# Kernel tuning notes

Measured on AMD Instinct MI355X. Metric: run time of the kernel, lower is better.

Reference implementation:

```python
import jax, jax.numpy as jnp
import numpy as np

B = 4
CTX = 2048
N_SUB = 16
RANK = 16
RANK_T = 16
LATENT = 256           # int(sqrt(CTX * N_SUB * 2))
T = 2 + 2 * RANK_T     # 34 transformation channels
H = 768
WD = 768
EPS = 1e-12
ASYM = 1e-4


def bgn(x):
    # backward_gradient_normalization: identity in the forward pass
    return x


def siglog(x):
    return jnp.sign(x) * jnp.log1p(jnp.abs(x))


def cmul(a, b):
    re = a[..., 0] * b[..., 0] - a[..., 1] * b[..., 1]
    im = a[..., 0] * b[..., 1] + a[..., 1] * b[..., 0]
    return jnp.stack([re, im], axis=-1)


def cdiv(a, b, eps):
    den = jnp.maximum(b[..., 0] ** 2 + b[..., 1] ** 2, eps)
    re = (a[..., 0] * b[..., 0] + a[..., 1] * b[..., 1]) / den
    im = (a[..., 1] * b[..., 0] - a[..., 0] * b[..., 1]) / den
    return jnp.stack([re, im], axis=-1)


def interp_linear(x, out_size):
    # x: [B, C, L] -> [B, C, out_size]; torch 'linear', align_corners=False
    L = x.shape[-1]
    pos = (jnp.arange(out_size, dtype=jnp.float32) + 0.5) * (L / out_size) - 0.5
    pos = jnp.clip(pos, 0.0, L - 1)
    lo = jnp.floor(pos).astype(jnp.int32)
    hi = jnp.minimum(lo + 1, L - 1)
    w = (pos - lo).astype(x.dtype)
    return x[..., lo] * (1.0 - w) + x[..., hi] * w


def transform_space(space, shift, z, size):
    # space [1,C,R,size,2], shift [B,C,R,2], z [B,Rt,C,R,2]
    sp = space + shift[:, :, :, None, :]
    bz = shift.shape[0]
    zt = jnp.transpose(z, (0, 4, 2, 3, 1)).reshape(bz, 2 * N_SUB * RANK, RANK_T)
    zt = interp_linear(zt, size)
    zt = jnp.transpose(zt.reshape(bz, 2, N_SUB, RANK, size), (0, 2, 3, 4, 1))
    return cmul(sp, zt)


def _forward(x, Wc, bc, space_i, space_j, inversions, G_Re, G_Im, w_mix, projections):
    xt = bgn(x @ Wc.T + bc)                        # [B, 4*LATENT]
    sl = LATENT * 2
    xm = (xt[:, :sl] * siglog(xt[:, sl:])).reshape(-1, LATENT, 2)
    GR, GI = bgn(G_Re), bgn(G_Im)
    xr, xi = xm[..., 0], xm[..., 1]
    Re = jnp.einsum('bl,tclr->btcr', xr, GR) - jnp.einsum('bl,tclr->btcr', xi, GI)
    Im = jnp.einsum('bl,tclr->btcr', xr, GI) + jnp.einsum('bl,tclr->btcr', xi, GR)
    shp = (Re.shape[0], T, N_SUB, LATENT, RANK)
    Re = bgn(jnp.broadcast_to(Re[:, :, :, None, :], shp))
    Im = bgn(jnp.broadcast_to(Im[:, :, :, None, :], shp))
    mag = jnp.sqrt(Re ** 2 + Im ** 2 + EPS)
    cos_t, sin_t = Re / mag, Im / mag
    msum = mag.sum(axis=3) + EPS
    cos_w = (cos_t * mag).sum(axis=3) / msum
    sin_w = (sin_t * mag).sum(axis=3) / msum
    mm = mag.mean(axis=3)
    trans = jnp.stack([cos_w * mm, sin_w * mm], axis=-1)   # [B,T,C,R,2]
    si = transform_space(bgn(space_i), trans[:, 0], trans[:, 2:2 + RANK_T], H)
    sj = transform_space(bgn(space_j), trans[:, 1], trans[:, 2 + RANK_T:2 + 2 * RANK_T], WD)
    inv = bgn(inversions)
    gI = cmul(si, inv)                                      # [B,C,R,H,2]
    gJ = cdiv(jnp.broadcast_to(inv, sj.shape), sj, ASYM)    # [B,C,R,W,2]
    wm = bgn(w_mix)
    tRe = jnp.einsum('bl,lk->bk', xr, wm[..., 0]) - jnp.einsum('bl,lk->bk', xi, wm[..., 1])
    tIm = jnp.einsum('bl,lk->bk', xr, wm[..., 1]) + jnp.einsum('bl,lk->bk', xi, wm[..., 0])
    beta = jax.nn.softmax(jnp.sqrt(tRe ** 2 + tIm ** 2 + EPS).reshape(-1, N_SUB, RANK), axis=-1)
    beta = beta[..., None, None]
    gI = (beta * gI).sum(axis=2)                            # [B,C,H,2]
    gJ = (beta * gJ).sum(axis=2)                            # [B,C,W,2]
    w_Re = jnp.einsum('bch,bcw->bchw', gI[..., 0], gJ[..., 0]) - jnp.einsum('bch,bcw->bchw', gI[..., 1], gJ[..., 1])
    w_Im = jnp.einsum('bch,bcw->bchw', gI[..., 0], gJ[..., 1]) + jnp.einsum('bch,bcw->bchw', gI[..., 1], gJ[..., 0])
    proj = bgn(projections)
    den = jnp.sqrt(jnp.sum(proj ** 2, axis=-1) + EPS)       # [1,C,H,W]
    pc, ps = proj[..., 0] / den, proj[..., 1] / den
    weights = w_Re * pc + w_Im * ps                         # [B,C,H,W]
    return weights.sum(axis=1)                              # [B,H,W]


def setup_inputs() -> dict:
    key = jax.random.key(0)
    ks = jax.random.split(key, 12)
    lim = 1.0 / np.sqrt(CTX)
    x = jax.random.normal(ks[0], (B, CTX), jnp.float32)
    Wc = jax.random.uniform(ks[1], (LATENT * 4, CTX), jnp.float32, -lim, lim)
    bc = jax.random.uniform(ks[2], (LATENT * 4,), jnp.float32, -lim, lim)
    space_i = jax.random.uniform(ks[3], (1, N_SUB, RANK, H, 2), jnp.float32, -1.0, 1.0)
    space_j = jax.random.uniform(ks[4], (1, N_SUB, RANK, WD, 2), jnp.float32, -1.0, 1.0)
    inversions = jax.random.uniform(ks[5], (1, N_SUB, 1, 1, 2), jnp.float32, -1.0, 1.0)
    gx = float(np.sqrt(6.0 / (N_SUB * LATENT * RANK + T * LATENT * RANK)))
    G_Re = jax.random.uniform(ks[6], (T, N_SUB, LATENT, RANK), jnp.float32, -gx, gx)
    G_Im = jax.random.uniform(ks[7], (T, N_SUB, LATENT, RANK), jnp.float32, -gx, gx)
    w_mix = jnp.stack([jnp.ones((LATENT, N_SUB * RANK), jnp.float32),
                       jnp.zeros((LATENT, N_SUB * RANK), jnp.float32)], axis=-1)
    pr = jax.random.gamma(ks[8], 0.5, (1, N_SUB, H, WD))
    pr = pr / (jnp.sum(pr, axis=-1, keepdims=True))         # Dirichlet(0.5) over last dim
    pi = jax.random.normal(ks[9], (1, N_SUB, H, WD)) * 0.001
    projections = jnp.stack([pr, pi], axis=-1).astype(jnp.float32)
    return {"x": x, "Wc": Wc, "bc": bc, "space_i": space_i, "space_j": space_j,
            "inversions": inversions, "G_Re": G_Re, "G_Im": G_Im,
            "w_mix": w_mix, "projections": projections}


def reference(x, Wc, bc, space_i, space_j, inversions, G_Re, G_Im, w_mix, projections):
    return _forward(x, Wc, bc, space_i, space_j, inversions, G_Re, G_Im, w_mix, projections)
```

## Files before the change

kernel.cpp:

```cpp
#include <hip/hip_runtime.h>
#include <math.h>

#define NCTX 2048
#define NT 34

typedef float f4 __attribute__((ext_vector_type(4)));
typedef float f2 __attribute__((ext_vector_type(2)));

#define OFF_XR 0u
#define OFF_XI 1024u
#define OFF_TR 2048u
#define OFF_GI 71680u
#define OFF_GJ 169984u

__device__ __forceinline__ float siglog(float v) {
  return copysignf(log1pf(fabsf(v)), v);
}

__device__ __forceinline__ f4 ntload4(const float* p) {
  return __builtin_nontemporal_load((const f4*)p);
}

__global__ __launch_bounds__(256) void k1_xm(const float* __restrict__ x,
                                             const float* __restrict__ Wc,
                                             const float* __restrict__ bc,
                                             float* __restrict__ xr,
                                             float* __restrict__ xi) {
  const int p = blockIdx.x;
  const int tid = threadIdx.x;
  const float* w1 = Wc + (size_t)p * NCTX;
  const float* w2 = Wc + (size_t)(p + 512) * NCTX;
  const f4* x4 = (const f4*)x;
  float a00 = 0.f, a01 = 0.f, a02 = 0.f, a03 = 0.f;
  float a10 = 0.f, a11 = 0.f, a12 = 0.f, a13 = 0.f;
  #pragma unroll
  for (int it = 0; it < 2; ++it) {
    int i = tid + it * 256;
    f4 wa = ntload4(w1 + i * 4);
    f4 wb = ntload4(w2 + i * 4);
    f4 v0 = x4[i];
    f4 v1 = x4[512 + i];
    f4 v2 = x4[1024 + i];
    f4 v3 = x4[1536 + i];
    a00 += wa.x * v0.x + wa.y * v0.y + wa.z * v0.z + wa.w * v0.w;
    a01 += wa.x * v1.x + wa.y * v1.y + wa.z * v1.z + wa.w * v1.w;
    a02 += wa.x * v2.x + wa.y * v2.y + wa.z * v2.z + wa.w * v2.w;
    a03 += wa.x * v3.x + wa.y * v3.y + wa.z * v3.z + wa.w * v3.w;
    a10 += wb.x * v0.x + wb.y * v0.y + wb.z * v0.z + wb.w * v0.w;
    a11 += wb.x * v1.x + wb.y * v1.y + wb.z * v1.z + wb.w * v1.w;
    a12 += wb.x * v2.x + wb.y * v2.y + wb.z * v2.z + wb.w * v2.w;
    a13 += wb.x * v3.x + wb.y * v3.y + wb.z * v3.z + wb.w * v3.w;
  }
  __shared__ float red[8][256];
  __shared__ float sums[8];
  red[0][tid] = a00; red[1][tid] = a01; red[2][tid] = a02; red[3][tid] = a03;
  red[4][tid] = a10; red[5][tid] = a11; red[6][tid] = a12; red[7][tid] = a13;
  __syncthreads();
  const int wv = tid >> 6, lane = tid & 63;
  #pragma unroll
  for (int q = 0; q < 2; ++q) {
    int combo = wv * 2 + q;
    float s = red[combo][lane] + red[combo][lane + 64] +
              red[combo][lane + 128] + red[combo][lane + 192];
    #pragma unroll
    for (int off = 32; off > 0; off >>= 1) s += __shfl_down(s, off, 64);
    if (lane == 0) sums[combo] = s;
  }
  __syncthreads();
  if (tid < 4) {
    float d1 = sums[tid] + bc[p];
    float d2 = sums[4 + tid] + bc[p + 512];
    float v = d1 * siglog(d2);
    float* dst = (p & 1) ? xi : xr;
    dst[tid * 256 + (p >> 1)] = v;
  }
}

__global__ __launch_bounds__(256) void k3_trans(const float* __restrict__ GR,
                                                const float* __restrict__ GIm,
                                                const float* __restrict__ xr,
                                                const float* __restrict__ xi,
                                                float* __restrict__ tr) {
  const int t = blockIdx.x >> 4;
  const int c = blockIdx.x & 15;
  const int tid = threadIdx.x;
  __shared__ float grT[16][260];
  __shared__ float giT[16][260];
  __shared__ float xr_s[1024];
  __shared__ float xi_s[1024];
  __shared__ float2 red2[4][64];
  const float* grp = GR + (size_t)(t * 16 + c) * 4096;
  const float* gip = GIm + (size_t)(t * 16 + c) * 4096;
  #pragma unroll
  for (int it = 0; it < 4; ++it) {
    int k = tid + it * 256;
    int l = k >> 2, q = (k & 3) * 4;
    f4 g = ntload4(grp + k * 4);
    grT[q + 0][l] = g.x; grT[q + 1][l] = g.y; grT[q + 2][l] = g.z; grT[q + 3][l] = g.w;
    f4 h = ntload4(gip + k * 4);
    giT[q + 0][l] = h.x; giT[q + 1][l] = h.y; giT[q + 2][l] = h.z; giT[q + 3][l] = h.w;
  }
  ((f4*)xr_s)[tid] = ((const f4*)xr)[tid];
  ((f4*)xi_s)[tid] = ((const f4*)xi)[tid];
  __syncthreads();
  const int r = tid & 15, b = (tid >> 4) & 3, lseg = tid >> 6;
  const f4* grv = (const f4*)&grT[r][lseg * 64];
  const f4* giv = (const f4*)&giT[r][lseg * 64];
  const f4* xrv = (const f4*)&xr_s[b * 256 + lseg * 64];
  const f4* xiv = (const f4*)&xi_s[b * 256 + lseg * 64];
  float are = 0.f, aim = 0.f;
  #pragma unroll
  for (int li = 0; li < 16; ++li) {
    f4 g = grv[li], gg = giv[li], vr = xrv[li], vi = xiv[li];
    are += vr.x * g.x - vi.x * gg.x;  aim += vr.x * gg.x + vi.x * g.x;
    are += vr.y * g.y - vi.y * gg.y;  aim += vr.y * gg.y + vi.y * g.y;
    are += vr.z * g.z - vi.z * gg.z;  aim += vr.z * gg.z + vi.z * g.z;
    are += vr.w * g.w - vi.w * gg.w;  aim += vr.w * gg.w + vi.w * g.w;
  }
  red2[lseg][b * 16 + r] = make_float2(are, aim);
  __syncthreads();
  if (tid < 64) {
    const int rr = tid & 15, bb = tid >> 4;
    float2 s0 = red2[0][tid], s1 = red2[1][tid], s2 = red2[2][tid], s3 = red2[3][tid];
    float sre = s0.x + s1.x + s2.x + s3.x;
    float sim = s0.y + s1.y + s2.y + s3.y;
    float mag = sqrtf(sre * sre + sim * sim + 1e-12f);
    float scale = 256.f * mag / (256.f * mag + 1e-12f);
    size_t o = ((((size_t)bb * NT + t) * 16 + c) * 16 + rr) * 2;
    tr[o]     = sre * scale;
    tr[o + 1] = sim * scale;
  }
}

__global__ __launch_bounds__(256) void k5_g(const float* __restrict__ space_i,
                                            const float* __restrict__ space_j,
                                            const float* __restrict__ invs,
                                            const float* __restrict__ tr,
                                            const float* __restrict__ xr,
                                            const float* __restrict__ xi,
                                            const float* __restrict__ wm,
                                            float* __restrict__ gI,
                                            float* __restrict__ gJ) {
  const int c = blockIdx.x, b = blockIdx.y;
  const int which = blockIdx.z / 3, seg = blockIdx.z % 3;
  const int tid = threadIdx.x;
  __shared__ float xr_s[256], xi_s[256];
  __shared__ float2 redb[16][16];
  __shared__ float sh_beta[16];
  __shared__ float sh_shift[16][2];
  __shared__ float sh_z[16][16][2];
  xr_s[tid] = xr[b * 256 + tid];
  xi_s[tid] = xi[b * 256 + tid];
  if (tid < 32) {
    int r = tid >> 1, comp = tid & 1;
    sh_shift[r][comp] = tr[((((size_t)b * NT + which) * 16 + c) * 16 + r) * 2 + comp];
  }
  for (int idx = tid; idx < 512; idx += 256) {
    int rt = idx >> 5, r = (idx >> 1) & 15, comp = idx & 1;
    int t = 2 + which * 16 + rt;
    sh_z[rt][r][comp] = tr[((((size_t)b * NT + t) * 16 + c) * 16 + r) * 2 + comp];
  }
  __syncthreads();
  {
    const int r = tid & 15, lseg = tid >> 4;
    const float2* wm2 = (const float2*)wm;
    float tre = 0.f, tim = 0.f;
    #pragma unroll
    for (int li = 0; li < 16; ++li) {
      int l = lseg * 16 + li;
      float2 w = wm2[(size_t)l * 256 + c * 16 + r];
      float vr = xr_s[l], vi = xi_s[l];
      tre += vr * w.x - vi * w.y;
      tim += vr * w.y + vi * w.x;
    }
    redb[lseg][r] = make_float2(tre, tim);
  }
  __syncthreads();
  if (tid < 16) {
    float sr = 0.f, si = 0.f;
    #pragma unroll
    for (int s = 0; s < 16; ++s) { sr += redb[s][tid].x; si += redb[s][tid].y; }
    float val = sqrtf(sr * sr + si * si + 1e-12f);
    float m = val;
    #pragma unroll
    for (int off = 8; off > 0; off >>= 1) m = fmaxf(m, __shfl_xor(m, off, 16));
    float e = expf(val - m);
    float ss = e;
    #pragma unroll
    for (int off = 8; off > 0; off >>= 1) ss += __shfl_xor(ss, off, 16);
    sh_beta[tid] = e / ss;
  }
  const float inv_re = invs[c * 2], inv_im = invs[c * 2 + 1];
  __syncthreads();
  const float2* sp2 = (const float2*)(which == 0 ? space_i : space_j);
  sp2 += (size_t)c * 16 * 768;
  float2* gout = (float2*)(which == 0 ? gI : gJ);
  gout += (size_t)(b * 16 + c) * 768;
  const int h = seg * 256 + tid;
  float pos = ((float)h + 0.5f) * (16.f / 768.f) - 0.5f;
  pos = fminf(fmaxf(pos, 0.f), 15.f);
  int lo = (int)floorf(pos);
  int hi = min(lo + 1, 15);
  float w = pos - (float)lo;
  float accR = 0.f, accI = 0.f;
  #pragma unroll
  for (int r = 0; r < 16; ++r) {
    float2 sp = sp2[r * 768 + h];
    float spr = sp.x + sh_shift[r][0];
    float spi = sp.y + sh_shift[r][1];
    float ztr = sh_z[lo][r][0] * (1.f - w) + sh_z[hi][r][0] * w;
    float zti = sh_z[lo][r][1] * (1.f - w) + sh_z[hi][r][1] * w;
    float sre = spr * ztr - spi * zti;
    float sim = spr * zti + spi * ztr;
    float br = sh_beta[r];
    if (which == 0) {
      accR += br * sre;
      accI += br * sim;
    } else {
      float den = fmaxf(sre * sre + sim * sim, 1e-4f);
      float id = 1.f / den;
      accR += br * (inv_re * sre + inv_im * sim) * id;
      accI += br * (inv_im * sre - inv_re * sim) * id;
    }
  }
  float2 o;
  if (which == 0) {
    o.x = accR * inv_re - accI * inv_im;
    o.y = accR * inv_im + accI * inv_re;
  } else {
    o.x = accR; o.y = accI;
  }
  gout[h] = o;
}

__global__ __launch_bounds__(256) void k6_out(const float* __restrict__ proj,
                                              const float* __restrict__ gI,
                                              const float* __restrict__ gJ,
                                              float* __restrict__ out) {
  const int w0 = blockIdx.x * 32;
  const int h0 = blockIdx.y * 32;
  const int tid = threadIdx.x;
  const int tw = tid & 15, th = tid >> 4;
  __shared__ float2 gIs[64][32];
  __shared__ float2 gJs[64][32];
  const float2* gI2 = (const float2*)gI;
  const float2* gJ2 = (const float2*)gJ;
  #pragma unroll
  for (int it = 0; it < 8; ++it) {
    int idx = tid + it * 256;
    int i = idx & 31, bcp = idx >> 5;
    gIs[bcp][i] = gI2[(size_t)bcp * 768 + h0 + i];
    gJs[bcp][i] = gJ2[(size_t)bcp * 768 + w0 + i];
  }
  __syncthreads();
  const float* pp = proj + ((size_t)(h0 + th * 2) * 384 + (w0 >> 1) + tw) * 4;
  float acc[4][4];
  #pragma unroll
  for (int b = 0; b < 4; ++b)
    #pragma unroll
    for (int q = 0; q < 4; ++q) acc[b][q] = 0.f;

  f4 pa = ntload4(pp);
  f4 pb = ntload4(pp + 384 * 4);
  #pragma unroll 1
  for (int c = 0; c < 16; ++c) {
    f4 c0 = pa, c1 = pb;
    if (c < 15) {
      size_t nxt = (size_t)(c + 1) * 768 * 384 * 4;
      pa = ntload4(pp + nxt);
      pb = ntload4(pp + nxt + 384 * 4);
    }
    float rq00 = rsqrtf(c0.x * c0.x + c0.y * c0.y + 1e-12f);
    float rq01 = rsqrtf(c0.z * c0.z + c0.w * c0.w + 1e-12f);
    float rq10 = rsqrtf(c1.x * c1.x + c1.y * c1.y + 1e-12f);
    float rq11 = rsqrtf(c1.z * c1.z + c1.w * c1.w + 1e-12f);
    float pr00 = c0.x * rq00, pi00 = c0.y * rq00;
    float pr01 = c0.z * rq01, pi01 = c0.w * rq01;
    float pr10 = c1.x * rq10, pi10 = c1.y * rq10;
    float pr11 = c1.z * rq11, pi11 = c1.w * rq11;
    #pragma unroll
    for (int b = 0; b < 4; ++b) {
      float2 gi0 = gIs[b * 16 + c][th * 2];
      float2 gi1 = gIs[b * 16 + c][th * 2 + 1];
      float2 gj0 = gJs[b * 16 + c][tw * 2];
      float2 gj1 = gJs[b * 16 + c][tw * 2 + 1];
      acc[b][0] += (gi0.x * gj0.x - gi0.y * gj0.y) * pr00 + (gi0.x * gj0.y + gi0.y * gj0.x) * pi00;
      acc[b][1] += (gi0.x * gj1.x - gi0.y * gj1.y) * pr01 + (gi0.x * gj1.y + gi0.y * gj1.x) * pi01;
      acc[b][2] += (gi1.x * gj0.x - gi1.y * gj0.y) * pr10 + (gi1.x * gj0.y + gi1.y * gj0.x) * pi10;
      acc[b][3] += (gi1.x * gj1.x - gi1.y * gj1.y) * pr11 + (gi1.x * gj1.y + gi1.y * gj1.x) * pi11;
    }
  }
  #pragma unroll
  for (int b = 0; b < 4; ++b) {
    #pragma unroll
    for (int hh = 0; hh < 2; ++hh) {
      int h = h0 + th * 2 + hh;
      f2 st;
      st.x = acc[b][hh * 2 + 0];
      st.y = acc[b][hh * 2 + 1];
      __builtin_nontemporal_store(st,
          (f2*)(out + (((size_t)b * 768 + h) * 384 + (w0 >> 1) + tw) * 2));
    }
  }
}

extern "C" void kernel_launch(void* const* d_in, const int* in_sizes, int n_in,
                              void* d_out, int out_size, void* d_ws, size_t ws_size,
                              hipStream_t stream) {
  (void)in_sizes; (void)n_in; (void)out_size; (void)ws_size;
  const float* x    = (const float*)d_in[0];
  const float* Wc   = (const float*)d_in[1];
  const float* bc   = (const float*)d_in[2];
  const float* spi  = (const float*)d_in[3];
  const float* spj  = (const float*)d_in[4];
  const float* invs = (const float*)d_in[5];
  const float* GR   = (const float*)d_in[6];
  const float* GIm  = (const float*)d_in[7];
  const float* wm   = (const float*)d_in[8];
  const float* proj = (const float*)d_in[9];
  float* out = (float*)d_out;
  float* ws  = (float*)d_ws;

  k1_xm   <<<512, 256, 0, stream>>>(x, Wc, bc, ws + OFF_XR, ws + OFF_XI);
  k3_trans<<<NT * 16, 256, 0, stream>>>(GR, GIm, ws + OFF_XR, ws + OFF_XI, ws + OFF_TR);
  k5_g    <<<dim3(16, 4, 6), 256, 0, stream>>>(spi, spj, invs, ws + OFF_TR,
                                               ws + OFF_XR, ws + OFF_XI, wm,
                                               ws + OFF_GI, ws + OFF_GJ);
  k6_out  <<<dim3(24, 24), 256, 0, stream>>>(proj, ws + OFF_GI, ws + OFF_GJ, out);
}
```

Baseline: 42.90 us.

## Fuse g-vector generation into output kernel and merge beta into trans kernel

Removes the separate k5_g kernel. The beta softmax computation now runs as extra blocks of the transformation kernel, and each output tile recomputes its own gI/gJ slices per channel from space, tr and beta held in shared memory. This saves one launch and the gI/gJ round trip through global memory. In exchange, every one of the 576 output blocks redundantly reloads tr per channel, adds two syncthreads per channel iteration, and recomputes the space products. The proj prefetch depth grows to two channels ahead.

```diff
diff --git a/kernel.cpp b/kernel.cpp
--- a/kernel.cpp
+++ b/kernel.cpp
@@ -10,8 +10,7 @@
 #define OFF_XR 0u
 #define OFF_XI 1024u
 #define OFF_TR 2048u
-#define OFF_GI 71680u
-#define OFF_GJ 169984u
+#define OFF_BE 71680u
 
 __device__ __forceinline__ float siglog(float v) {
   return copysignf(log1pf(fabsf(v)), v);
@@ -21,7 +20,7 @@
   return __builtin_nontemporal_load((const f4*)p);
 }
 
-__global__ __launch_bounds__(256) void k1_xm(const float* __restrict__ x,
+__global__ __launch_bounds__(256) void n1_xm(const float* __restrict__ x,
                                              const float* __restrict__ Wc,
                                              const float* __restrict__ bc,
                                              float* __restrict__ xr,
@@ -76,220 +75,240 @@
   }
 }
 
-__global__ __launch_bounds__(256) void k3_trans(const float* __restrict__ GR,
-                                                const float* __restrict__ GIm,
-                                                const float* __restrict__ xr,
-                                                const float* __restrict__ xi,
-                                                float* __restrict__ tr) {
-  const int t = blockIdx.x >> 4;
-  const int c = blockIdx.x & 15;
+__global__ __launch_bounds__(256) void n2_trans_beta(
+    const float* __restrict__ GR, const float* __restrict__ GIm,
+    const float* __restrict__ xr, const float* __restrict__ xi,
+    const float* __restrict__ wm, float* __restrict__ tr,
+    float* __restrict__ beta) {
+  const int u = blockIdx.x;
   const int tid = threadIdx.x;
-  __shared__ float grT[16][260];
-  __shared__ float giT[16][260];
-  __shared__ float xr_s[1024];
-  __shared__ float xi_s[1024];
-  __shared__ float2 red2[4][64];
-  const float* grp = GR + (size_t)(t * 16 + c) * 4096;
-  const float* gip = GIm + (size_t)(t * 16 + c) * 4096;
-  #pragma unroll
-  for (int it = 0; it < 4; ++it) {
-    int k = tid + it * 256;
-    int l = k >> 2, q = (k & 3) * 4;
-    f4 g = ntload4(grp + k * 4);
-    grT[q + 0][l] = g.x; grT[q + 1][l] = g.y; grT[q + 2][l] = g.z; grT[q + 3][l] = g.w;
-    f4 h = ntload4(gip + k * 4);
-    giT[q + 0][l] = h.x; giT[q + 1][l] = h.y; giT[q + 2][l] = h.z; giT[q + 3][l] = h.w;
-  }
-  ((f4*)xr_s)[tid] = ((const f4*)xr)[tid];
-  ((f4*)xi_s)[tid] = ((const f4*)xi)[tid];
-  __syncthreads();
-  const int r = tid & 15, b = (tid >> 4) & 3, lseg = tid >> 6;
-  const f4* grv = (const f4*)&grT[r][lseg * 64];
-  const f4* giv = (const f4*)&giT[r][lseg * 64];
-  const f4* xrv = (const f4*)&xr_s[b * 256 + lseg * 64];
-  const f4* xiv = (const f4*)&xi_s[b * 256 + lseg * 64];
-  float are = 0.f, aim = 0.f;
-  #pragma unroll
-  for (int li = 0; li < 16; ++li) {
-    f4 g = grv[li], gg = giv[li], vr = xrv[li], vi = xiv[li];
-    are += vr.x * g.x - vi.x * gg.x;  aim += vr.x * gg.x + vi.x * g.x;
-    are += vr.y * g.y - vi.y * gg.y;  aim += vr.y * gg.y + vi.y * g.y;
-    are += vr.z * g.z - vi.z * gg.z;  aim += vr.z * gg.z + vi.z * g.z;
-    are += vr.w * g.w - vi.w * gg.w;  aim += vr.w * gg.w + vi.w * g.w;
-  }
-  red2[lseg][b * 16 + r] = make_float2(are, aim);
-  __syncthreads();
-  if (tid < 64) {
-    const int rr = tid & 15, bb = tid >> 4;
-    float2 s0 = red2[0][tid], s1 = red2[1][tid], s2 = red2[2][tid], s3 = red2[3][tid];
-    float sre = s0.x + s1.x + s2.x + s3.x;
-    float sim = s0.y + s1.y + s2.y + s3.y;
-    float mag = sqrtf(sre * sre + sim * sim + 1e-12f);
-    float scale = 256.f * mag / (256.f * mag + 1e-12f);
-    size_t o = ((((size_t)bb * NT + t) * 16 + c) * 16 + rr) * 2;
-    tr[o]     = sre * scale;
-    tr[o + 1] = sim * scale;
-  }
-}
-
-__global__ __launch_bounds__(256) void k5_g(const float* __restrict__ space_i,
-                                            const float* __restrict__ space_j,
-                                            const float* __restrict__ invs,
-                                            const float* __restrict__ tr,
-                                            const float* __restrict__ xr,
-                                            const float* __restrict__ xi,
-                                            const float* __restrict__ wm,
-                                            float* __restrict__ gI,
-                                            float* __restrict__ gJ) {
-  const int c = blockIdx.x, b = blockIdx.y;
-  const int which = blockIdx.z / 3, seg = blockIdx.z % 3;
-  const int tid = threadIdx.x;
-  __shared__ float xr_s[256], xi_s[256];
-  __shared__ float2 redb[16][16];
-  __shared__ float sh_beta[16];
-  __shared__ float sh_shift[16][2];
-  __shared__ float sh_z[16][16][2];
-  xr_s[tid] = xr[b * 256 + tid];
-  xi_s[tid] = xi[b * 256 + tid];
-  if (tid < 32) {
-    int r = tid >> 1, comp = tid & 1;
-    sh_shift[r][comp] = tr[((((size_t)b * NT + which) * 16 + c) * 16 + r) * 2 + comp];
-  }
-  for (int idx = tid; idx < 512; idx += 256) {
-    int rt = idx >> 5, r = (idx >> 1) & 15, comp = idx & 1;
-    int t = 2 + which * 16 + rt;
-    sh_z[rt][r][comp] = tr[((((size_t)b * NT + t) * 16 + c) * 16 + r) * 2 + comp];
-  }
-  __syncthreads();
-  {
+  __shared__ __align__(16) float smem[10880];
+  if (u < NT * 16) {
+    const int t = u >> 4;
+    const int c = u & 15;
+    float* grT = smem;
+    float* giT = smem + 4160;
+    float* xr_s = smem + 8320;
+    float* xi_s = smem + 9344;
+    f2* red2 = (f2*)(smem + 10368);
+    const float* grp = GR + (size_t)(t * 16 + c) * 4096;
+    const float* gip = GIm + (size_t)(t * 16 + c) * 4096;
+    #pragma unroll
+    for (int it = 0; it < 4; ++it) {
+      int k = tid + it * 256;
+      int l = k >> 2, q = (k & 3) * 4;
+      f4 g = ntload4(grp + k * 4);
+      grT[(q + 0) * 260 + l] = g.x; grT[(q + 1) * 260 + l] = g.y;
+      grT[(q + 2) * 260 + l] = g.z; grT[(q + 3) * 260 + l] = g.w;
+      f4 h = ntload4(gip + k * 4);
+      giT[(q + 0) * 260 + l] = h.x; giT[(q + 1) * 260 + l] = h.y;
+      giT[(q + 2) * 260 + l] = h.z; giT[(q + 3) * 260 + l] = h.w;
+    }
+    ((f4*)xr_s)[tid] = ((const f4*)xr)[tid];
+    ((f4*)xi_s)[tid] = ((const f4*)xi)[tid];
+    __syncthreads();
+    const int r = tid & 15, b = (tid >> 4) & 3, lseg = tid >> 6;
+    const f4* grv = (const f4*)&grT[r * 260 + lseg * 64];
+    const f4* giv = (const f4*)&giT[r * 260 + lseg * 64];
+    const f4* xrv = (const f4*)&xr_s[b * 256 + lseg * 64];
+    const f4* xiv = (const f4*)&xi_s[b * 256 + lseg * 64];
+    float are = 0.f, aim = 0.f;
+    #pragma unroll
+    for (int li = 0; li < 16; ++li) {
+      f4 g = grv[li], gg = giv[li], vr = xrv[li], vi = xiv[li];
+      are += vr.x * g.x - vi.x * gg.x;  aim += vr.x * gg.x + vi.x * g.x;
+      are += vr.y * g.y - vi.y * gg.y;  aim += vr.y * gg.y + vi.y * g.y;
+      are += vr.z * g.z - vi.z * gg.z;  aim += vr.z * gg.z + vi.z * g.z;
+      are += vr.w * g.w - vi.w * gg.w;  aim += vr.w * gg.w + vi.w * g.w;
+    }
+    f2 rv; rv.x = are; rv.y = aim;
+    red2[lseg * 64 + b * 16 + r] = rv;
+    __syncthreads();
+    if (tid < 64) {
+      const int rr = tid & 15, bb = tid >> 4;
+      f2 s0 = red2[0 * 64 + tid], s1 = red2[1 * 64 + tid];
+      f2 s2 = red2[2 * 64 + tid], s3 = red2[3 * 64 + tid];
+      float sre = s0.x + s1.x + s2.x + s3.x;
+      float sim = s0.y + s1.y + s2.y + s3.y;
+      float mag = sqrtf(sre * sre + sim * sim + 1e-12f);
+      float scale = 256.f * mag / (256.f * mag + 1e-12f);
+      size_t o = ((((size_t)bb * NT + t) * 16 + c) * 16 + rr) * 2;
+      tr[o]     = sre * scale;
+      tr[o + 1] = sim * scale;
+    }
+  } else {
+    const int u2 = u - NT * 16;
+    const int n = u2 & 15, b = u2 >> 4;
+    float* xr_s = smem;
+    float* xi_s = smem + 256;
+    f2* redb = (f2*)(smem + 512);
+    {
+      int l = tid;
+      xr_s[l] = xr[b * 256 + l];
+      xi_s[l] = xi[b * 256 + l];
+    }
+    __syncthreads();
     const int r = tid & 15, lseg = tid >> 4;
-    const float2* wm2 = (const float2*)wm;
+    const f2* wm2 = (const f2*)wm;
     float tre = 0.f, tim = 0.f;
     #pragma unroll
     for (int li = 0; li < 16; ++li) {
       int l = lseg * 16 + li;
-      float2 w = wm2[(size_t)l * 256 + c * 16 + r];
+      f2 w = wm2[(size_t)l * 256 + n * 16 + r];
       float vr = xr_s[l], vi = xi_s[l];
       tre += vr * w.x - vi * w.y;
       tim += vr * w.y + vi * w.x;
     }
-    redb[lseg][r] = make_float2(tre, tim);
-  }
-  __syncthreads();
-  if (tid < 16) {
-    float sr = 0.f, si = 0.f;
-    #pragma unroll
-    for (int s = 0; s < 16; ++s) { sr += redb[s][tid].x; si += redb[s][tid].y; }
-    float val = sqrtf(sr * sr + si * si + 1e-12f);
-    float m = val;
-    #pragma unroll
-    for (int off = 8; off > 0; off >>= 1) m = fmaxf(m, __shfl_xor(m, off, 16));
-    float e = expf(val - m);
-    float ss = e;
-    #pragma unroll
-    for (int off = 8; off > 0; off >>= 1) ss += __shfl_xor(ss, off, 16);
-    sh_beta[tid] = e / ss;
-  }
-  const float inv_re = invs[c * 2], inv_im = invs[c * 2 + 1];
-  __syncthreads();
-  const float2* sp2 = (const float2*)(which == 0 ? space_i : space_j);
-  sp2 += (size_t)c * 16 * 768;
-  float2* gout = (float2*)(which == 0 ? gI : gJ);
-  gout += (size_t)(b * 16 + c) * 768;
-  const int h = seg * 256 + tid;
-  float pos = ((float)h + 0.5f) * (16.f / 768.f) - 0.5f;
-  pos = fminf(fmaxf(pos, 0.f), 15.f);
-  int lo = (int)floorf(pos);
-  int hi = min(lo + 1, 15);
-  float w = pos - (float)lo;
-  float accR = 0.f, accI = 0.f;
-  #pragma unroll
-  for (int r = 0; r < 16; ++r) {
-    float2 sp = sp2[r * 768 + h];
-    float spr = sp.x + sh_shift[r][0];
-    float spi = sp.y + sh_shift[r][1];
-    float ztr = sh_z[lo][r][0] * (1.f - w) + sh_z[hi][r][0] * w;
-    float zti = sh_z[lo][r][1] * (1.f - w) + sh_z[hi][r][1] * w;
-    float sre = spr * ztr - spi * zti;
-    float sim = spr * zti + spi * ztr;
-    float br = sh_beta[r];
-    if (which == 0) {
-      accR += br * sre;
-      accI += br * sim;
-    } else {
-      float den = fmaxf(sre * sre + sim * sim, 1e-4f);
-      float id = 1.f / den;
-      accR += br * (inv_re * sre + inv_im * sim) * id;
-      accI += br * (inv_im * sre - inv_re * sim) * id;
-    }
-  }
-  float2 o;
-  if (which == 0) {
-    o.x = accR * inv_re - accI * inv_im;
-    o.y = accR * inv_im + accI * inv_re;
-  } else {
-    o.x = accR; o.y = accI;
-  }
-  gout[h] = o;
-}
-
-__global__ __launch_bounds__(256) void k6_out(const float* __restrict__ proj,
-                                              const float* __restrict__ gI,
-                                              const float* __restrict__ gJ,
-                                              float* __restrict__ out) {
-  const int w0 = blockIdx.x * 32;
-  const int h0 = blockIdx.y * 32;
+    f2 rv; rv.x = tre; rv.y = tim;
+    redb[lseg * 16 + r] = rv;
+    __syncthreads();
+    if (tid < 16) {
+      float sr = 0.f, si = 0.f;
+      #pragma unroll
+      for (int s = 0; s < 16; ++s) { sr += redb[s * 16 + tid].x; si += redb[s * 16 + tid].y; }
+      float val = sqrtf(sr * sr + si * si + 1e-12f);
+      float m = val;
+      #pragma unroll
+      for (int off = 8; off > 0; off >>= 1) m = fmaxf(m, __shfl_xor(m, off, 16));
+      float e = expf(val - m);
+      float ss = e;
+      #pragma unroll
+      for (int off = 8; off > 0; off >>= 1) ss += __shfl_xor(ss, off, 16);
+      beta[(b * 16 + n) * 16 + tid] = e / ss;
+    }
+  }
+}
+
+__global__ __launch_bounds__(256) void n3_out(
+    const float* __restrict__ space_i, const float* __restrict__ space_j,
+    const float* __restrict__ invs, const float* __restrict__ tr,
+    const float* __restrict__ beta, const float* __restrict__ proj,
+    float* __restrict__ out) {
+  const int u = blockIdx.x;
+  const int w0 = (u % 24) * 32;
+  const int h0 = (u / 24) * 32;
   const int tid = threadIdx.x;
   const int tw = tid & 15, th = tid >> 4;
-  __shared__ float2 gIs[64][32];
-  __shared__ float2 gJs[64][32];
-  const float2* gI2 = (const float2*)gI;
-  const float2* gJ2 = (const float2*)gJ;
-  #pragma unroll
-  for (int it = 0; it < 8; ++it) {
-    int idx = tid + it * 256;
-    int i = idx & 31, bcp = idx >> 5;
-    gIs[bcp][i] = gI2[(size_t)bcp * 768 + h0 + i];
-    gJs[bcp][i] = gJ2[(size_t)bcp * 768 + w0 + i];
-  }
-  __syncthreads();
-  const float* pp = proj + ((size_t)(h0 + th * 2) * 384 + (w0 >> 1) + tw) * 4;
+  __shared__ f2 lds_tr[4][NT][16];
+  __shared__ float lds_beta[4][16][16];
+  __shared__ f2 lds_inv[16];
+  __shared__ f2 gIt[4][32];
+  __shared__ f2 gJt[4][32];
+
+  for (int idx = tid; idx < 1024; idx += 256) lds_beta[idx >> 8][(idx >> 4) & 15][idx & 15] = beta[idx];
+  if (tid < 16) lds_inv[tid] = ((const f2*)invs)[tid];
+
   float acc[4][4];
   #pragma unroll
   for (int b = 0; b < 4; ++b)
     #pragma unroll
     for (int q = 0; q < 4; ++q) acc[b][q] = 0.f;
 
-  f4 pa = ntload4(pp);
-  f4 pb = ntload4(pp + 384 * 4);
+  const float* ppbase = proj + ((size_t)(h0 + th * 2) * 384 + (w0 >> 1) + tw) * 4;
+  const size_t CSTRIDE = (size_t)768 * 384 * 4;
+  f4 pa0 = ntload4(ppbase);
+  f4 pb0 = ntload4(ppbase + 384 * 4);
+  f4 pa1 = ntload4(ppbase + CSTRIDE);
+  f4 pb1 = ntload4(ppbase + CSTRIDE + 384 * 4);
+
+  const int side = tid >> 7;
+  const int bb = (tid >> 5) & 3;
+  const int p = tid & 31;
+  const int hw = (side == 0 ? h0 : w0) + p;
+  float pos = ((float)hw + 0.5f) * (16.f / 768.f) - 0.5f;
+  pos = fminf(fmaxf(pos, 0.f), 15.f);
+  const int lo = (int)floorf(pos);
+  const int hi = min(lo + 1, 15);
+  const float lw = pos - (float)lo;
+  const f2* spbase = (const f2*)(side == 0 ? space_i : space_j);
+
   #pragma unroll 1
   for (int c = 0; c < 16; ++c) {
-    f4 c0 = pa, c1 = pb;
-    if (c < 15) {
-      size_t nxt = (size_t)(c + 1) * 768 * 384 * 4;
-      pa = ntload4(pp + nxt);
-      pb = ntload4(pp + nxt + 384 * 4);
-    }
-    float rq00 = rsqrtf(c0.x * c0.x + c0.y * c0.y + 1e-12f);
-    float rq01 = rsqrtf(c0.z * c0.z + c0.w * c0.w + 1e-12f);
-    float rq10 = rsqrtf(c1.x * c1.x + c1.y * c1.y + 1e-12f);
-    float rq11 = rsqrtf(c1.z * c1.z + c1.w * c1.w + 1e-12f);
-    float pr00 = c0.x * rq00, pi00 = c0.y * rq00;
-    float pr01 = c0.z * rq01, pi01 = c0.w * rq01;
-    float pr10 = c1.x * rq10, pi10 = c1.y * rq10;
-    float pr11 = c1.z * rq11, pi11 = c1.w * rq11;
-    #pragma unroll
-    for (int b = 0; b < 4; ++b) {
-      float2 gi0 = gIs[b * 16 + c][th * 2];
-      float2 gi1 = gIs[b * 16 + c][th * 2 + 1];
-      float2 gj0 = gJs[b * 16 + c][tw * 2];
-      float2 gj1 = gJs[b * 16 + c][tw * 2 + 1];
-      acc[b][0] += (gi0.x * gj0.x - gi0.y * gj0.y) * pr00 + (gi0.x * gj0.y + gi0.y * gj0.x) * pi00;
-      acc[b][1] += (gi0.x * gj1.x - gi0.y * gj1.y) * pr01 + (gi0.x * gj1.y + gi0.y * gj1.x) * pi01;
-      acc[b][2] += (gi1.x * gj0.x - gi1.y * gj0.y) * pr10 + (gi1.x * gj0.y + gi1.y * gj0.x) * pi10;
-      acc[b][3] += (gi1.x * gj1.x - gi1.y * gj1.y) * pr11 + (gi1.x * gj1.y + gi1.y * gj1.x) * pi11;
-    }
-  }
+    const f2* tr2 = (const f2*)tr;
+    for (int idx = tid; idx < 4 * NT * 16; idx += 256) {
+      int b = idx / (NT * 16);
+      int rem = idx - b * NT * 16;
+      int t = rem >> 4, r = rem & 15;
+      lds_tr[b][t][r] = tr2[(((size_t)b * NT + t) * 16 + c) * 16 + r];
+    }
+    __syncthreads();
+    {
+      f2 sh = lds_tr[bb][side][0];
+      (void)sh;
+      float accR = 0.f, accI = 0.f;
+      const int tz = 2 + side * 16;
+      const f2* sp = spbase + ((size_t)c * 16) * 768 + hw;
+      const f2 inv = lds_inv[c];
+      #pragma unroll
+      for (int r = 0; r < 16; ++r) {
+        f2 spv = sp[r * 768];
+        f2 shf = lds_tr[bb][side][r];
+        float spr = spv.x + shf.x;
+        float spi = spv.y + shf.y;
+        f2 zl = lds_tr[bb][tz + lo][r];
+        f2 zh = lds_tr[bb][tz + hi][r];
+        float ztr = zl.x * (1.f - lw) + zh.x * lw;
+        float zti = zl.y * (1.f - lw) + zh.y * lw;
+        float sre = spr * ztr - spi * zti;
+        float sim = spr * zti + spi * ztr;
+        float br = lds_beta[bb][c][r];
+        if (side == 0) {
+          accR += br * sre;
+          accI += br * sim;
+        } else {
+          float den = fmaxf(sre * sre + sim * sim, 1e-4f);
+          float id = 1.f / den;
+          accR += br * (inv.x * sre + inv.y * sim) * id;
+          accI += br * (inv.y * sre - inv.x * sim) * id;
+        }
+      }
+      f2 o;
+      if (side == 0) {
+        o.x = accR * inv.x - accI * inv.y;
+        o.y = accR * inv.y + accI * inv.x;
+        gIt[bb][p] = o;
+      } else {
+        o.x = accR; o.y = accI;
+        gJt[bb][p] = o;
+      }
+    }
+    __syncthreads();
+    f4 pa2, pb2;
+    bool have2 = (c + 2 < 16);
+    if (have2) {
+      pa2 = ntload4(ppbase + (size_t)(c + 2) * CSTRIDE);
+      pb2 = ntload4(ppbase + (size_t)(c + 2) * CSTRIDE + 384 * 4);
+    }
+    {
+      f4 c0 = pa0, c1 = pb0;
+      float rq00 = rsqrtf(c0.x * c0.x + c0.y * c0.y + 1e-12f);
+      float rq01 = rsqrtf(c0.z * c0.z + c0.w * c0.w + 1e-12f);
+      float rq10 = rsqrtf(c1.x * c1.x + c1.y * c1.y + 1e-12f);
+      float rq11 = rsqrtf(c1.z * c1.z + c1.w * c1.w + 1e-12f);
+      float pr00 = c0.x * rq00, pi00 = c0.y * rq00;
+      float pr01 = c0.z * rq01, pi01 = c0.w * rq01;
+      float pr10 = c1.x * rq10, pi10 = c1.y * rq10;
+      float pr11 = c1.z * rq11, pi11 = c1.w * rq11;
+      #pragma unroll
+      for (int b = 0; b < 4; ++b) {
+        f2 gi0 = gIt[b][th * 2];
+        f2 gi1 = gIt[b][th * 2 + 1];
+        f2 gj0 = gJt[b][tw * 2];
+        f2 gj1 = gJt[b][tw * 2 + 1];
+        acc[b][0] += (gi0.x * gj0.x - gi0.y * gj0.y) * pr00 +
+                     (gi0.x * gj0.y + gi0.y * gj0.x) * pi00;
+        acc[b][1] += (gi0.x * gj1.x - gi0.y * gj1.y) * pr01 +
+                     (gi0.x * gj1.y + gi0.y * gj1.x) * pi01;
+        acc[b][2] += (gi1.x * gj0.x - gi1.y * gj0.y) * pr10 +
+                     (gi1.x * gj0.y + gi1.y * gj0.x) * pi10;
+        acc[b][3] += (gi1.x * gj1.x - gi1.y * gj1.y) * pr11 +
+                     (gi1.x * gj1.y + gi1.y * gj1.x) * pi11;
+      }
+    }
+    pa0 = pa1; pb0 = pb1;
+    pa1 = pa2; pb1 = pb2;
+  }
+
   #pragma unroll
   for (int b = 0; b < 4; ++b) {
     #pragma unroll
@@ -321,10 +340,9 @@
   float* out = (float*)d_out;
   float* ws  = (float*)d_ws;
 
-  k1_xm   <<<512, 256, 0, stream>>>(x, Wc, bc, ws + OFF_XR, ws + OFF_XI);
-  k3_trans<<<NT * 16, 256, 0, stream>>>(GR, GIm, ws + OFF_XR, ws + OFF_XI, ws + OFF_TR);
-  k5_g    <<<dim3(16, 4, 6), 256, 0, stream>>>(spi, spj, invs, ws + OFF_TR,
-                                               ws + OFF_XR, ws + OFF_XI, wm,
-                                               ws + OFF_GI, ws + OFF_GJ);
-  k6_out  <<<dim3(24, 24), 256, 0, stream>>>(proj, ws + OFF_GI, ws + OFF_GJ, out);
-}
+  n1_xm        <<<512, 256, 0, stream>>>(x, Wc, bc, ws + OFF_XR, ws + OFF_XI);
+  n2_trans_beta<<<NT * 16 + 64, 256, 0, stream>>>(GR, GIm, ws + OFF_XR, ws + OFF_XI,
+                                                  wm, ws + OFF_TR, ws + OFF_BE);
+  n3_out       <<<576, 256, 0, stream>>>(spi, spj, invs, ws + OFF_TR, ws + OFF_BE,
+                                         proj, out);
+}
```

New measurement: 122.7 us. +186.0%, slower.

## Move beta softmax into trans kernel and deepen projection prefetch in output kernel

Applied to the files above, without the earlier changes.

The per-(b,c) beta softmax over w_mix is now computed once in 64 extra blocks of the transformation kernel and stored in workspace. Previously it was recomputed redundantly by each of the six k5_g blocks that share a (b,c), which shortens k5_g's serial prologue. The output kernel's projection stream now keeps four channels of loads in flight in a register ring instead of one, with the loop unrolled by four. The cost is more registers in k6_out and a larger grid for the combined kernel.

```diff
diff --git a/kernel.cpp b/kernel.cpp
--- a/kernel.cpp
+++ b/kernel.cpp
@@ -10,8 +10,9 @@
 #define OFF_XR 0u
 #define OFF_XI 1024u
 #define OFF_TR 2048u
-#define OFF_GI 71680u
-#define OFF_GJ 169984u
+#define OFF_BE 71680u
+#define OFF_GI 72704u
+#define OFF_GJ 171008u
 
 __device__ __forceinline__ float siglog(float v) {
   return copysignf(log1pf(fabsf(v)), v);
@@ -21,7 +22,7 @@
   return __builtin_nontemporal_load((const f4*)p);
 }
 
-__global__ __launch_bounds__(256) void k1_xm(const float* __restrict__ x,
+__global__ __launch_bounds__(256) void n1_xm(const float* __restrict__ x,
                                              const float* __restrict__ Wc,
                                              const float* __restrict__ bc,
                                              float* __restrict__ xr,
@@ -76,59 +77,104 @@
   }
 }
 
-__global__ __launch_bounds__(256) void k3_trans(const float* __restrict__ GR,
-                                                const float* __restrict__ GIm,
-                                                const float* __restrict__ xr,
-                                                const float* __restrict__ xi,
-                                                float* __restrict__ tr) {
-  const int t = blockIdx.x >> 4;
-  const int c = blockIdx.x & 15;
+__global__ __launch_bounds__(256) void n2_trans_beta(
+    const float* __restrict__ GR, const float* __restrict__ GIm,
+    const float* __restrict__ xr, const float* __restrict__ xi,
+    const float* __restrict__ wm, float* __restrict__ tr,
+    float* __restrict__ beta) {
+  const int u = blockIdx.x;
   const int tid = threadIdx.x;
-  __shared__ float grT[16][260];
-  __shared__ float giT[16][260];
-  __shared__ float xr_s[1024];
-  __shared__ float xi_s[1024];
-  __shared__ float2 red2[4][64];
-  const float* grp = GR + (size_t)(t * 16 + c) * 4096;
-  const float* gip = GIm + (size_t)(t * 16 + c) * 4096;
-  #pragma unroll
-  for (int it = 0; it < 4; ++it) {
-    int k = tid + it * 256;
-    int l = k >> 2, q = (k & 3) * 4;
-    f4 g = ntload4(grp + k * 4);
-    grT[q + 0][l] = g.x; grT[q + 1][l] = g.y; grT[q + 2][l] = g.z; grT[q + 3][l] = g.w;
-    f4 h = ntload4(gip + k * 4);
-    giT[q + 0][l] = h.x; giT[q + 1][l] = h.y; giT[q + 2][l] = h.z; giT[q + 3][l] = h.w;
-  }
-  ((f4*)xr_s)[tid] = ((const f4*)xr)[tid];
-  ((f4*)xi_s)[tid] = ((const f4*)xi)[tid];
-  __syncthreads();
-  const int r = tid & 15, b = (tid >> 4) & 3, lseg = tid >> 6;
-  const f4* grv = (const f4*)&grT[r][lseg * 64];
-  const f4* giv = (const f4*)&giT[r][lseg * 64];
-  const f4* xrv = (const f4*)&xr_s[b * 256 + lseg * 64];
-  const f4* xiv = (const f4*)&xi_s[b * 256 + lseg * 64];
-  float are = 0.f, aim = 0.f;
-  #pragma unroll
-  for (int li = 0; li < 16; ++li) {
-    f4 g = grv[li], gg = giv[li], vr = xrv[li], vi = xiv[li];
-    are += vr.x * g.x - vi.x * gg.x;  aim += vr.x * gg.x + vi.x * g.x;
-    are += vr.y * g.y - vi.y * gg.y;  aim += vr.y * gg.y + vi.y * g.y;
-    are += vr.z * g.z - vi.z * gg.z;  aim += vr.z * gg.z + vi.z * g.z;
-    are += vr.w * g.w - vi.w * gg.w;  aim += vr.w * gg.w + vi.w * g.w;
-  }
-  red2[lseg][b * 16 + r] = make_float2(are, aim);
-  __syncthreads();
-  if (tid < 64) {
-    const int rr = tid & 15, bb = tid >> 4;
-    float2 s0 = red2[0][tid], s1 = red2[1][tid], s2 = red2[2][tid], s3 = red2[3][tid];
-    float sre = s0.x + s1.x + s2.x + s3.x;
-    float sim = s0.y + s1.y + s2.y + s3.y;
-    float mag = sqrtf(sre * sre + sim * sim + 1e-12f);
-    float scale = 256.f * mag / (256.f * mag + 1e-12f);
-    size_t o = ((((size_t)bb * NT + t) * 16 + c) * 16 + rr) * 2;
-    tr[o]     = sre * scale;
-    tr[o + 1] = sim * scale;
+  __shared__ __align__(16) float smem[10880];
+  if (u < NT * 16) {
+    const int t = u >> 4;
+    const int c = u & 15;
+    float* grT = smem;
+    float* giT = smem + 4160;
+    float* xr_s = smem + 8320;
+    float* xi_s = smem + 9344;
+    f2* red2 = (f2*)(smem + 10368);
+    const float* grp = GR + (size_t)(t * 16 + c) * 4096;
+    const float* gip = GIm + (size_t)(t * 16 + c) * 4096;
+    #pragma unroll
+    for (int it = 0; it < 4; ++it) {
+      int k = tid + it * 256;
+      int l = k >> 2, q = (k & 3) * 4;
+      f4 g = ntload4(grp + k * 4);
+      grT[(q + 0) * 260 + l] = g.x; grT[(q + 1) * 260 + l] = g.y;
+      grT[(q + 2) * 260 + l] = g.z; grT[(q + 3) * 260 + l] = g.w;
+      f4 h = ntload4(gip + k * 4);
+      giT[(q + 0) * 260 + l] = h.x; giT[(q + 1) * 260 + l] = h.y;
+      giT[(q + 2) * 260 + l] = h.z; giT[(q + 3) * 260 + l] = h.w;
+    }
+    ((f4*)xr_s)[tid] = ((const f4*)xr)[tid];
+    ((f4*)xi_s)[tid] = ((const f4*)xi)[tid];
+    __syncthreads();
+    const int r = tid & 15, b = (tid >> 4) & 3, lseg = tid >> 6;
+    const f4* grv = (const f4*)&grT[r * 260 + lseg * 64];
+    const f4* giv = (const f4*)&giT[r * 260 + lseg * 64];
+    const f4* xrv = (const f4*)&xr_s[b * 256 + lseg * 64];
+    const f4* xiv = (const f4*)&xi_s[b * 256 + lseg * 64];
+    float are = 0.f, aim = 0.f;
+    #pragma unroll
+    for (int li = 0; li < 16; ++li) {
+      f4 g = grv[li], gg = giv[li], vr = xrv[li], vi = xiv[li];
+      are += vr.x * g.x - vi.x * gg.x;  aim += vr.x * gg.x + vi.x * g.x;
+      are += vr.y * g.y - vi.y * gg.y;  aim += vr.y * gg.y + vi.y * g.y;
+      are += vr.z * g.z - vi.z * gg.z;  aim += vr.z * gg.z + vi.z * g.z;
+      are += vr.w * g.w - vi.w * gg.w;  aim += vr.w * gg.w + vi.w * g.w;
+    }
+    f2 rv; rv.x = are; rv.y = aim;
+    red2[lseg * 64 + b * 16 + r] = rv;
+    __syncthreads();
+    if (tid < 64) {
+      const int rr = tid & 15, bb = tid >> 4;
+      f2 s0 = red2[0 * 64 + tid], s1 = red2[1 * 64 + tid];
+      f2 s2 = red2[2 * 64 + tid], s3 = red2[3 * 64 + tid];
+      float sre = s0.x + s1.x + s2.x + s3.x;
+      float sim = s0.y + s1.y + s2.y + s3.y;
+      float mag = sqrtf(sre * sre + sim * sim + 1e-12f);
+      float scale = 256.f * mag / (256.f * mag + 1e-12f);
+      size_t o = ((((size_t)bb * NT + t) * 16 + c) * 16 + rr) * 2;
+      tr[o]     = sre * scale;
+      tr[o + 1] = sim * scale;
+    }
+  } else {
+    const int u2 = u - NT * 16;
+    const int n = u2 & 15, b = u2 >> 4;
+    float* xr_s = smem;
+    float* xi_s = smem + 256;
+    f2* redb = (f2*)(smem + 512);
+    xr_s[tid] = xr[b * 256 + tid];
+    xi_s[tid] = xi[b * 256 + tid];
+    __syncthreads();
+    const int r = tid & 15, lseg = tid >> 4;
+    const f2* wm2 = (const f2*)wm;
+    float tre = 0.f, tim = 0.f;
+    #pragma unroll
+    for (int li = 0; li < 16; ++li) {
+      int l = lseg * 16 + li;
+      f2 w = wm2[(size_t)l * 256 + n * 16 + r];
+      float vr = xr_s[l], vi = xi_s[l];
+      tre += vr * w.x - vi * w.y;
+      tim += vr * w.y + vi * w.x;
+    }
+    f2 rv; rv.x = tre; rv.y = tim;
+    redb[lseg * 16 + r] = rv;
+    __syncthreads();
+    if (tid < 16) {
+      float sr = 0.f, si = 0.f;
+      #pragma unroll
+      for (int s = 0; s < 16; ++s) { sr += redb[s * 16 + tid].x; si += redb[s * 16 + tid].y; }
+      float val = sqrtf(sr * sr + si * si + 1e-12f);
+      float m = val;
+      #pragma unroll
+      for (int off = 8; off > 0; off >>= 1) m = fmaxf(m, __shfl_xor(m, off, 16));
+      float e = expf(val - m);
+      float ss = e;
+      #pragma unroll
+      for (int off = 8; off > 0; off >>= 1) ss += __shfl_xor(ss, off, 16);
+      beta[(b * 16 + n) * 16 + tid] = e / ss;
+    }
   }
 }
 
@@ -136,23 +182,19 @@
                                             const float* __restrict__ space_j,
                                             const float* __restrict__ invs,
                                             const float* __restrict__ tr,
-                                            const float* __restrict__ xr,
-                                            const float* __restrict__ xi,
-                                            const float* __restrict__ wm,
+                                            const float* __restrict__ beta,
                                             float* __restrict__ gI,
                                             float* __restrict__ gJ) {
   const int c = blockIdx.x, b = blockIdx.y;
   const int which = blockIdx.z / 3, seg = blockIdx.z % 3;
   const int tid = threadIdx.x;
-  __shared__ float xr_s[256], xi_s[256];
-  __shared__ float2 redb[16][16];
   __shared__ float sh_beta[16];
   __shared__ float sh_shift[16][2];
   __shared__ float sh_z[16][16][2];
-  xr_s[tid] = xr[b * 256 + tid];
-  xi_s[tid] = xi[b * 256 + tid];
-  if (tid < 32) {
-    int r = tid >> 1, comp = tid & 1;
+  if (tid < 16) sh_beta[tid] = beta[(b * 16 + c) * 16 + tid];
+  if (tid >= 32 && tid < 64) {
+    int t2 = tid - 32;
+    int r = t2 >> 1, comp = t2 & 1;
     sh_shift[r][comp] = tr[((((size_t)b * NT + which) * 16 + c) * 16 + r) * 2 + comp];
   }
   for (int idx = tid; idx < 512; idx += 256) {
@@ -160,41 +202,11 @@
     int t = 2 + which * 16 + rt;
     sh_z[rt][r][comp] = tr[((((size_t)b * NT + t) * 16 + c) * 16 + r) * 2 + comp];
   }
-  __syncthreads();
-  {
-    const int r = tid & 15, lseg = tid >> 4;
-    const float2* wm2 = (const float2*)wm;
-    float tre = 0.f, tim = 0.f;
-    #pragma unroll
-    for (int li = 0; li < 16; ++li) {
-      int l = lseg * 16 + li;
-      float2 w = wm2[(size_t)l * 256 + c * 16 + r];
-      float vr = xr_s[l], vi = xi_s[l];
-      tre += vr * w.x - vi * w.y;
-      tim += vr * w.y + vi * w.x;
-    }
-    redb[lseg][r] = make_float2(tre, tim);
-  }
-  __syncthreads();
-  if (tid < 16) {
-    float sr = 0.f, si = 0.f;
-    #pragma unroll
-    for (int s = 0; s < 16; ++s) { sr += redb[s][tid].x; si += redb[s][tid].y; }
-    float val = sqrtf(sr * sr + si * si + 1e-12f);
-    float m = val;
-    #pragma unroll
-    for (int off = 8; off > 0; off >>= 1) m = fmaxf(m, __shfl_xor(m, off, 16));
-    float e = expf(val - m);
-    float ss = e;
-    #pragma unroll
-    for (int off = 8; off > 0; off >>= 1) ss += __shfl_xor(ss, off, 16);
-    sh_beta[tid] = e / ss;
-  }
   const float inv_re = invs[c * 2], inv_im = invs[c * 2 + 1];
   __syncthreads();
-  const float2* sp2 = (const float2*)(which == 0 ? space_i : space_j);
+  const f2* sp2 = (const f2*)(which == 0 ? space_i : space_j);
   sp2 += (size_t)c * 16 * 768;
-  float2* gout = (float2*)(which == 0 ? gI : gJ);
+  f2* gout = (f2*)(which == 0 ? gI : gJ);
   gout += (size_t)(b * 16 + c) * 768;
   const int h = seg * 256 + tid;
   float pos = ((float)h + 0.5f) * (16.f / 768.f) - 0.5f;
@@ -205,7 +217,7 @@
   float accR = 0.f, accI = 0.f;
   #pragma unroll
   for (int r = 0; r < 16; ++r) {
-    float2 sp = sp2[r * 768 + h];
+    f2 sp = sp2[r * 768 + h];
     float spr = sp.x + sh_shift[r][0];
     float spi = sp.y + sh_shift[r][1];
     float ztr = sh_z[lo][r][0] * (1.f - w) + sh_z[hi][r][0] * w;
@@ -223,7 +235,7 @@
       accI += br * (inv_im * sre - inv_re * sim) * id;
     }
   }
-  float2 o;
+  f2 o;
   if (which == 0) {
     o.x = accR * inv_re - accI * inv_im;
     o.y = accR * inv_im + accI * inv_re;
@@ -241,10 +253,10 @@
   const int h0 = blockIdx.y * 32;
   const int tid = threadIdx.x;
   const int tw = tid & 15, th = tid >> 4;
-  __shared__ float2 gIs[64][32];
-  __shared__ float2 gJs[64][32];
-  const float2* gI2 = (const float2*)gI;
-  const float2* gJ2 = (const float2*)gJ;
+  __shared__ f2 gIs[64][32];
+  __shared__ f2 gJs[64][32];
+  const f2* gI2 = (const f2*)gI;
+  const f2* gJ2 = (const f2*)gJ;
   #pragma unroll
   for (int it = 0; it < 8; ++it) {
     int idx = tid + it * 256;
@@ -254,21 +266,25 @@
   }
   __syncthreads();
   const float* pp = proj + ((size_t)(h0 + th * 2) * 384 + (w0 >> 1) + tw) * 4;
+  const size_t CS = (size_t)768 * 384 * 4;
   float acc[4][4];
   #pragma unroll
   for (int b = 0; b < 4; ++b)
     #pragma unroll
     for (int q = 0; q < 4; ++q) acc[b][q] = 0.f;
 
-  f4 pa = ntload4(pp);
-  f4 pb = ntload4(pp + 384 * 4);
-  #pragma unroll 1
+  f4 ra[4], rb[4];
+  #pragma unroll
+  for (int i = 0; i < 4; ++i) {
+    ra[i] = ntload4(pp + (size_t)i * CS);
+    rb[i] = ntload4(pp + (size_t)i * CS + 384 * 4);
+  }
+  #pragma unroll 4
   for (int c = 0; c < 16; ++c) {
-    f4 c0 = pa, c1 = pb;
-    if (c < 15) {
-      size_t nxt = (size_t)(c + 1) * 768 * 384 * 4;
-      pa = ntload4(pp + nxt);
-      pb = ntload4(pp + nxt + 384 * 4);
+    f4 c0 = ra[c & 3], c1 = rb[c & 3];
+    if (c + 4 < 16) {
+      ra[c & 3] = ntload4(pp + (size_t)(c + 4) * CS);
+      rb[c & 3] = ntload4(pp + (size_t)(c + 4) * CS + 384 * 4);
     }
     float rq00 = rsqrtf(c0.x * c0.x + c0.y * c0.y + 1e-12f);
     float rq01 = rsqrtf(c0.z * c0.z + c0.w * c0.w + 1e-12f);
@@ -280,14 +296,18 @@
     float pr11 = c1.z * rq11, pi11 = c1.w * rq11;
     #pragma unroll
     for (int b = 0; b < 4; ++b) {
-      float2 gi0 = gIs[b * 16 + c][th * 2];
-      float2 gi1 = gIs[b * 16 + c][th * 2 + 1];
-      float2 gj0 = gJs[b * 16 + c][tw * 2];
-      float2 gj1 = gJs[b * 16 + c][tw * 2 + 1];
-      acc[b][0] += (gi0.x * gj0.x - gi0.y * gj0.y) * pr00 + (gi0.x * gj0.y + gi0.y * gj0.x) * pi00;
-      acc[b][1] += (gi0.x * gj1.x - gi0.y * gj1.y) * pr01 + (gi0.x * gj1.y + gi0.y * gj1.x) * pi01;
-      acc[b][2] += (gi1.x * gj0.x - gi1.y * gj0.y) * pr10 + (gi1.x * gj0.y + gi1.y * gj0.x) * pi10;
-      acc[b][3] += (gi1.x * gj1.x - gi1.y * gj1.y) * pr11 + (gi1.x * gj1.y + gi1.y * gj1.x) * pi11;
+      f2 gi0 = gIs[b * 16 + c][th * 2];
+      f2 gi1 = gIs[b * 16 + c][th * 2 + 1];
+      f2 gj0 = gJs[b * 16 + c][tw * 2];
+      f2 gj1 = gJs[b * 16 + c][tw * 2 + 1];
+      acc[b][0] += (gi0.x * gj0.x - gi0.y * gj0.y) * pr00 +
+                   (gi0.x * gj0.y + gi0.y * gj0.x) * pi00;
+      acc[b][1] += (gi0.x * gj1.x - gi0.y * gj1.y) * pr01 +
+                   (gi0.x * gj1.y + gi0.y * gj1.x) * pi01;
+      acc[b][2] += (gi1.x * gj0.x - gi1.y * gj0.y) * pr10 +
+                   (gi1.x * gj0.y + gi1.y * gj0.x) * pi10;
+      acc[b][3] += (gi1.x * gj1.x - gi1.y * gj1.y) * pr11 +
+                   (gi1.x * gj1.y + gi1.y * gj1.x) * pi11;
     }
   }
   #pragma unroll
@@ -321,10 +341,10 @@
   float* out = (float*)d_out;
   float* ws  = (float*)d_ws;
 
-  k1_xm   <<<512, 256, 0, stream>>>(x, Wc, bc, ws + OFF_XR, ws + OFF_XI);
-  k3_trans<<<NT * 16, 256, 0, stream>>>(GR, GIm, ws + OFF_XR, ws + OFF_XI, ws + OFF_TR);
-  k5_g    <<<dim3(16, 4, 6), 256, 0, stream>>>(spi, spj, invs, ws + OFF_TR,
-                                               ws + OFF_XR, ws + OFF_XI, wm,
-                                               ws + OFF_GI, ws + OFF_GJ);
-  k6_out  <<<dim3(24, 24), 256, 0, stream>>>(proj, ws + OFF_GI, ws + OFF_GJ, out);
-}
+  n1_xm        <<<512, 256, 0, stream>>>(x, Wc, bc, ws + OFF_XR, ws + OFF_XI);
+  n2_trans_beta<<<NT * 16 + 64, 256, 0, stream>>>(GR, GIm, ws + OFF_XR, ws + OFF_XI,
+                                                  wm, ws + OFF_TR, ws + OFF_BE);
+  k5_g         <<<dim3(16, 4, 6), 256, 0, stream>>>(spi, spj, invs, ws + OFF_TR,
+                                                    ws + OFF_BE, ws + OFF_GI, ws + OFF_GJ);
+  k6_out       <<<dim3(24, 24), 256, 0, stream>>>(proj, ws + OFF_GI, ws + OFF_GJ, out);
+}
```

New measurement: 51.21 us. 19.3% more time.
